# Performance work log

Measured on AMD Instinct MI355X. Metric: run time of the kernel, lower is better.

## Reference

```python
import jax, jax.numpy as jnp
import numpy as np

D_MODEL = 1024
N_HEADS = 16
N_GROUPS = 4
D_HEAD = D_MODEL // N_HEADS  # 64
HPG = N_HEADS // N_GROUPS    # heads per KV group = 4
B, T = 2, 2048


def _rope(x):
    # x: [B, H, T, D]; interleaved even/odd rotary, matching the torch module
    t, d = x.shape[2], x.shape[3]
    pos = jnp.arange(t, dtype=jnp.float32)[:, None]                      # [T,1]
    freq = jnp.exp(-(jnp.arange(0, d, 2, dtype=jnp.float32) / d)
                   * jnp.log(jnp.float32(10000.0)))                      # [D/2]
    angle = pos * freq                                                   # [T, D/2]
    cos, sin = jnp.cos(angle), jnp.sin(angle)
    xe, xo = x[..., ::2], x[..., 1::2]
    re = xe * cos - xo * sin
    ro = xe * sin + xo * cos
    return jnp.stack([re, ro], axis=-1).reshape(x.shape)


def setup_inputs() -> dict:
    key = jax.random.key(0)
    ks = jax.random.split(key, 10)
    s = 0.02
    return {
        "x":  jax.random.normal(ks[0], (B, T, D_MODEL), dtype=jnp.float32),
        "Wq": jax.random.normal(ks[1], (D_MODEL, D_MODEL), dtype=jnp.float32) * s,
        "bq": jax.random.normal(ks[2], (D_MODEL,), dtype=jnp.float32) * s,
        "Wk": jax.random.normal(ks[3], (D_MODEL, N_GROUPS * D_HEAD), dtype=jnp.float32) * s,
        "bk": jax.random.normal(ks[4], (N_GROUPS * D_HEAD,), dtype=jnp.float32) * s,
        "Wv": jax.random.normal(ks[5], (D_MODEL, N_GROUPS * D_HEAD), dtype=jnp.float32) * s,
        "bv": jax.random.normal(ks[6], (N_GROUPS * D_HEAD,), dtype=jnp.float32) * s,
        "Wo": jax.random.normal(ks[7], (D_MODEL, D_MODEL), dtype=jnp.float32) * s,
        "bo": jax.random.normal(ks[8], (D_MODEL,), dtype=jnp.float32) * s,
    }


def reference(x, Wq, bq, Wk, bk, Wv, bv, Wo, bo):
    b, t, _ = x.shape
    q = (x @ Wq + bq).reshape(b, t, N_HEADS, D_HEAD).transpose(0, 2, 1, 3)    # [B,H,T,D]
    k = (x @ Wk + bk).reshape(b, t, N_GROUPS, D_HEAD).transpose(0, 2, 1, 3)   # [B,G,T,D]
    v = (x @ Wv + bv).reshape(b, t, N_GROUPS, D_HEAD).transpose(0, 2, 1, 3)
    # GQA broadcast: idx = arange(n_heads) // heads_per_group  ==  repeat each group HPG times
    k = jnp.repeat(k, HPG, axis=1)                                            # [B,H,T,D]
    v = jnp.repeat(v, HPG, axis=1)
    q = _rope(q)
    k = _rope(k)
    scale = jnp.float32(np.sqrt(D_HEAD))
    scores = jnp.einsum('bhtd,bhsd->bhts', q, k) / scale                      # [B,H,T,T]
    causal = jnp.tril(jnp.ones((t, t), dtype=bool))
    scores = jnp.where(causal, scores, -jnp.inf)
    probs = jax.nn.softmax(scores, axis=-1)
    # dropout(p=0.05) is identity in eval mode
    attn = jnp.einsum('bhts,bhsd->bhtd', probs, v)
    out = attn.transpose(0, 2, 1, 3).reshape(b, t, N_HEADS * D_HEAD)
    return out @ Wo + bo
```

## Files before the change

### kernel.cpp

```cpp
#include <hip/hip_runtime.h>
#include <stdint.h>

typedef unsigned short u16;
typedef __attribute__((ext_vector_type(4))) float f32x4;
typedef __attribute__((ext_vector_type(8))) short bf16x8;
typedef __attribute__((ext_vector_type(4))) short bf16x4;

#define T_SEQ 2048
#define DM 1024
#define NH 16
#define NG 4
#define DH 64
#define QSCALE 0.18033688011112042f

__device__ __forceinline__ u16 f2bf(float f) {
    union { float f; uint32_t u; } v; v.f = f;
    uint32_t r = (v.u + 0x7FFFu + ((v.u >> 16) & 1u)) >> 16;
    return (u16)r;
}
__device__ __forceinline__ float bf2f(u16 u) {
    union { uint32_t u; float f; } v; v.u = ((uint32_t)u) << 16;
    return v.f;
}
__device__ __forceinline__ float fexp2(float x) {
#if __has_builtin(__builtin_amdgcn_exp2f)
    return __builtin_amdgcn_exp2f(x);
#else
    return exp2f(x);
#endif
}
__device__ __forceinline__ uint32_t cvtpk_bf16(float a, float b) {
    uint32_t r;
    asm("v_cvt_pk_bf16_f32 %0, %1, %2" : "=v"(r) : "v"(a), "v"(b));
    return r;
}

#if __has_builtin(__builtin_amdgcn_mfma_f32_16x16x16_bf16)
__device__ __forceinline__ f32x4 mfma16(bf16x4 a, bf16x4 b, f32x4 c) {
    return __builtin_amdgcn_mfma_f32_16x16x16_bf16(a, b, c, 0, 0, 0);
}
#elif __has_builtin(__builtin_amdgcn_mfma_f32_16x16x16bf16_1k)
__device__ __forceinline__ f32x4 mfma16(bf16x4 a, bf16x4 b, f32x4 c) {
    return __builtin_amdgcn_mfma_f32_16x16x16bf16_1k(a, b, c, 0, 0, 0);
}
#else
__device__ __forceinline__ f32x4 mfma16(bf16x4 a, bf16x4 b, f32x4 c) {
    asm("v_mfma_f32_16x16x16_bf16 %0, %1, %2, %0" : "+v"(c) : "v"(a), "v"(b));
    return c;
}
#endif

__device__ __forceinline__ void async16(const void* g, void* l) {
    __builtin_amdgcn_global_load_lds(
        (const __attribute__((address_space(1))) void*)g,
        (__attribute__((address_space(3))) void*)l,
        16, 0, 0);
}

__global__ __launch_bounds__(256) void k_prep(
    const float* __restrict__ x, u16* __restrict__ xb,
    const float* __restrict__ Wq, const float* __restrict__ Wk,
    const float* __restrict__ Wv, const float* __restrict__ Wo,
    u16* __restrict__ wqkvt, u16* __restrict__ wot,
    const float* __restrict__ bq, const float* __restrict__ bk,
    const float* __restrict__ bv, float* __restrict__ bqkv,
    float2* __restrict__ tbl) {
    int blk = blockIdx.x;
    int tid = threadIdx.x;
    if (blk < 2048) {
        int i = blk * 256 + tid;
        const float4* p = (const float4*)x + (size_t)i * 2;
        float4 a = p[0], b = p[1];
        bf16x8 v;
        v[0] = (short)f2bf(a.x); v[1] = (short)f2bf(a.y);
        v[2] = (short)f2bf(a.z); v[3] = (short)f2bf(a.w);
        v[4] = (short)f2bf(b.x); v[5] = (short)f2bf(b.y);
        v[6] = (short)f2bf(b.z); v[7] = (short)f2bf(b.w);
        ((bf16x8*)xb)[i] = v;
        return;
    }
    int t = blk - 2048;
    if (t >= 2560) {
        int u = t - 2560;
        if (u < 6) {
            int i = u * 256 + tid;
            if (i < 1536) {
                float v;
                if (i < 1024) v = bq[i];
                else if (i < 1280) v = bk[i - 1024];
                else v = bv[i - 1280];
                bqkv[i] = v;
            }
        } else {
            int idx = (u - 6) * 256 + tid;
            int tt = idx >> 5, i = idx & 31;
            float freq = exp2f(-(float)i * (13.287712379549449f / 32.0f));
            float ang = (float)tt * freq;
            tbl[idx] = make_float2(cosf(ang), sinf(ang));
        }
        return;
    }
    const float* src; u16* dst; int N;
    if (t < 1024)      { src = Wq; dst = wqkvt;                      N = 1024; }
    else if (t < 1280) { t -= 1024; src = Wk; dst = wqkvt + (size_t)1024 * 1024; N = 256; }
    else if (t < 1536) { t -= 1280; src = Wv; dst = wqkvt + (size_t)1280 * 1024; N = 256; }
    else               { t -= 1536; src = Wo; dst = wot;             N = 1024; }
    int ntiles = N >> 5;
    int n0 = (t % ntiles) * 32, k0 = (t / ntiles) * 32;
    __shared__ float tile[32][33];
    int tx = tid & 31, ty = tid >> 5;
#pragma unroll
    for (int q = 0; q < 4; q++)
        tile[ty + q * 8][tx] = src[(size_t)(k0 + ty + q * 8) * N + n0 + tx];
    __syncthreads();
#pragma unroll
    for (int q = 0; q < 4; q++)
        dst[(size_t)(n0 + ty + q * 8) * 1024 + k0 + tx] = f2bf(tile[tx][ty + q * 8]);
}

template <int EPI>
__global__ __launch_bounds__(256) void k_gemm(
    const u16* __restrict__ A, const u16* __restrict__ Bt,
    const float* __restrict__ bias, float* __restrict__ C,
    const float2* __restrict__ tbl, u16* __restrict__ Qo,
    u16* __restrict__ Ko, u16* __restrict__ Vto, int N, int K) {
    __shared__ __align__(16) u16 As[2][64 * 64];
    __shared__ __align__(16) u16 Bs[2][128 * 64];
    int tid = threadIdx.x;
    int lane = tid & 63, wid = tid >> 6;
    int wr = wid >> 1, wc = wid & 1;
    int l15 = lane & 15, lhi = lane >> 4;
    int row0 = blockIdx.y * 64, col0 = blockIdx.x * 128;
    f32x4 acc[2][4] = {};

    const u16* ga[2];
    const u16* gb[4];
#pragma unroll
    for (int i = 0; i < 2; i++) {
        int c = i * 256 + tid, r = c >> 3, sch = (c & 7) ^ (r & 7);
        ga[i] = A + (size_t)(row0 + r) * K + sch * 8;
    }
#pragma unroll
    for (int i = 0; i < 4; i++) {
        int c = i * 256 + tid, r = c >> 3, sch = (c & 7) ^ (r & 7);
        gb[i] = Bt + (size_t)(col0 + r) * K + sch * 8;
    }

#pragma unroll
    for (int i = 0; i < 2; i++) async16(ga[i], &As[0][(i * 256 + tid) * 8]);
#pragma unroll
    for (int i = 0; i < 4; i++) async16(gb[i], &Bs[0][(i * 256 + tid) * 8]);
    __syncthreads();

    int nk = K >> 6;
    for (int kt = 0; kt < nk; kt++) {
        int cur = kt & 1;
        if (kt + 1 < nk) {
            int nx = cur ^ 1, ko = (kt + 1) << 6;
#pragma unroll
            for (int i = 0; i < 2; i++) async16(ga[i] + ko, &As[nx][(i * 256 + tid) * 8]);
#pragma unroll
            for (int i = 0; i < 4; i++) async16(gb[i] + ko, &Bs[nx][(i * 256 + tid) * 8]);
        }
        const u16* Ac = As[cur];
        const u16* Bc = Bs[cur];
#pragma unroll
        for (int ks = 0; ks < 2; ks++) {
            bf16x8 af[2], bfr[4];
#pragma unroll
            for (int m = 0; m < 2; m++) {
                int r = wr * 32 + m * 16 + l15;
                int kb = (ks * 64 + lhi * 16) ^ ((r & 7) << 4);
                af[m] = *(const bf16x8*)((const char*)Ac + r * 128 + kb);
            }
#pragma unroll
            for (int n = 0; n < 4; n++) {
                int r = wc * 64 + n * 16 + l15;
                int kb = (ks * 64 + lhi * 16) ^ ((r & 7) << 4);
                bfr[n] = *(const bf16x8*)((const char*)Bc + r * 128 + kb);
            }
#pragma unroll
            for (int m = 0; m < 2; m++)
#pragma unroll
                for (int n = 0; n < 4; n++)
                    acc[m][n] = __builtin_amdgcn_mfma_f32_16x16x32_bf16(
                        af[m], bfr[n], acc[m][n], 0, 0, 0);
        }
        __syncthreads();
    }

    if (EPI == 0) {
#pragma unroll
        for (int n = 0; n < 4; n++) {
            int col = col0 + wc * 64 + n * 16 + l15;
            float bv = bias[col];
#pragma unroll
            for (int m = 0; m < 2; m++) {
                int row = row0 + wr * 32 + m * 16 + lhi * 4;
#pragma unroll
                for (int i = 0; i < 4; i++)
                    C[(size_t)(row + i) * N + col] = acc[m][n][i] + bv;
            }
        }
    } else {
        int type = (col0 >= 1280) ? 2 : (col0 >= 1024 ? 1 : 0);
        int rbase = row0 + wr * 32;
#pragma unroll
        for (int n = 0; n < 4; n++) {
            int col = col0 + wc * 64 + n * 16 + l15;
            float bv = bias[col];
            if (type == 2) {
                int cc = col - 1280;
                int g = cc >> 6, d = cc & 63;
#pragma unroll
                for (int m = 0; m < 2; m++)
#pragma unroll
                    for (int i = 0; i < 4; i++) {
                        int rowg = rbase + m * 16 + lhi * 4 + i;
                        int t = rowg & (T_SEQ - 1), b = rowg >> 11;
                        int sp = t ^ ((d & 1) << 2);
                        Vto[(((size_t)(b * NG + g)) * DH + d) * T_SEQ + sp] =
                            f2bf(acc[m][n][i] + bv);
                    }
            } else {
                float ssgn = (col & 1) ? 1.f : -1.f;
                int ip = (col & 63) >> 1;
#pragma unroll
                for (int m = 0; m < 2; m++)
#pragma unroll
                    for (int i = 0; i < 4; i++) {
                        int rowg = rbase + m * 16 + lhi * 4 + i;
                        int t = rowg & (T_SEQ - 1), b = rowg >> 11;
                        float v = acc[m][n][i] + bv;
                        float other = __shfl_xor(v, 1);
                        float2 cs = tbl[t * 32 + ip];
                        float out = v * cs.x + other * cs.y * ssgn;
                        if (type == 0) {
                            int h = col >> 6, d = col & 63;
                            Qo[(((size_t)(b * NH + h)) * T_SEQ + t) * DH + d] =
                                f2bf(out * QSCALE);
                        } else {
                            int cc = col - 1024;
                            int g = cc >> 6, d = cc & 63;
                            Ko[(((size_t)(b * NG + g)) * T_SEQ + t) * DH + d] = f2bf(out);
                        }
                    }
            }
        }
    }
}

__global__ __launch_bounds__(256) void k_attn(
    const u16* __restrict__ Q, const u16* __restrict__ K,
    const u16* __restrict__ Vt, u16* __restrict__ Aout) {
    int i0 = blockIdx.x;
    int u = i0 >> 5;
    int qt = (u < 16) ? (31 - u) : (u - 16);
    int bh = i0 & 31;
    int b = bh >> 4, h = bh & 15, g = h >> 2;
    int tid = threadIdx.x;
    int lane = tid & 63, wid = tid >> 6;
    int l15 = lane & 15, lhi = lane >> 4;

    const u16* Kp = K + ((size_t)(b * NG + g)) * T_SEQ * DH;
    const u16* Vp = Vt + ((size_t)(b * NG + g)) * DH * T_SEQ;

    __shared__ __align__(16) u16 Ks[2][64 * 64];
    __shared__ __align__(16) u16 Vs[2][64 * 64];

    const u16* Qp = Q + ((size_t)bh * T_SEQ + qt * 64) * DH;
    bf16x8 qf[2];
#pragma unroll
    for (int ks = 0; ks < 2; ks++)
        qf[ks] = *(const bf16x8*)(Qp + (size_t)(wid * 16 + l15) * DH + ks * 32 + lhi * 8);

    f32x4 of[4] = {};
    float m_i = -3.0e38f, l_i = 0.f;

    int nt = qt + 1;
    int swz = (l15 & 7) << 4;

    int c0 = tid, c1 = tid + 256;
    int rk0 = c0 >> 3, rk1 = c1 >> 3;
    int sk0 = (c0 & 7) ^ (rk0 & 7);
    int sk1 = (c1 & 7) ^ (rk1 & 7);
    int sv0 = (c0 & 7) ^ ((rk0 >> 1) & 7);
    int sv1 = (c1 & 7) ^ ((rk1 >> 1) & 7);
    const u16* kg0 = Kp + rk0 * DH + sk0 * 8;
    const u16* kg1 = Kp + rk1 * DH + sk1 * 8;
    const u16* vg0 = Vp + (size_t)rk0 * T_SEQ + sv0 * 8;
    const u16* vg1 = Vp + (size_t)rk1 * T_SEQ + sv1 * 8;

    async16(kg0, &Ks[0][c0 * 8]);
    async16(kg1, &Ks[0][c1 * 8]);
    async16(vg0, &Vs[0][c0 * 8]);
    async16(vg1, &Vs[0][c1 * 8]);
    __syncthreads();

#pragma unroll 1
    for (int it = 0; it < nt; it++) {
        int cur = it & 1;
        if (it + 1 < nt) {
            int nx = cur ^ 1;
            int ko = (it + 1) << 12;
            int vo = (it + 1) << 6;
            async16(kg0 + ko, &Ks[nx][c0 * 8]);
            async16(kg1 + ko, &Ks[nx][c1 * 8]);
            async16(vg0 + vo, &Vs[nx][c0 * 8]);
            async16(vg1 + vo, &Vs[nx][c1 * 8]);
        }
        const u16* Kc = Ks[cur];
        const u16* Vc = Vs[cur];

        f32x4 sf[4] = {};
        __builtin_amdgcn_s_setprio(1);
#pragma unroll
        for (int ks = 0; ks < 2; ks++)
#pragma unroll
            for (int n = 0; n < 4; n++) {
                int kb = (ks * 64 + lhi * 16) ^ swz;
                bf16x8 kf = *(const bf16x8*)((const char*)Kc + (n * 16 + l15) * 128 + kb);
                sf[n] = __builtin_amdgcn_mfma_f32_16x16x32_bf16(kf, qf[ks], sf[n], 0, 0, 0);
            }
        __builtin_amdgcn_s_setprio(0);

        if (it == nt - 1) {
            int qrow = qt * 64 + wid * 16 + l15;
            int sb = it * 64 + lhi * 4;
#pragma unroll
            for (int n = 0; n < 4; n++)
#pragma unroll
                for (int i = 0; i < 4; i++)
                    if (sb + n * 16 + i > qrow) sf[n][i] = -3.0e38f;
        }

        float pmt = sf[0][0];
#pragma unroll
        for (int n = 0; n < 4; n++)
#pragma unroll
            for (int i = 0; i < 4; i++)
                pmt = fmaxf(pmt, sf[n][i]);
        if (!__all(pmt - m_i <= 8.f)) {
#pragma unroll
            for (int off = 16; off <= 32; off <<= 1)
                pmt = fmaxf(pmt, __shfl_xor(pmt, off));
            float mn = fmaxf(m_i, pmt);
            float sc = fexp2(m_i - mn);
            m_i = mn;
            l_i *= sc;
            float sc4[4];
#pragma unroll
            for (int i = 0; i < 4; i++)
                sc4[i] = __shfl(sc, lhi * 4 + i);
#pragma unroll
            for (int n = 0; n < 4; n++)
#pragma unroll
                for (int i = 0; i < 4; i++)
                    of[n][i] *= sc4[i];
        }
        bf16x4 pa[4];
#pragma unroll
        for (int n = 0; n < 4; n++) {
#pragma unroll
            for (int i = 0; i < 4; i++) {
                float p = fexp2(sf[n][i] - m_i);
                sf[n][i] = p;
                l_i += p;
            }
            union { uint32_t uu[2]; bf16x4 v; } pu;
            pu.uu[0] = cvtpk_bf16(sf[n][0], sf[n][1]);
            pu.uu[1] = cvtpk_bf16(sf[n][2], sf[n][3]);
            pa[n] = pu.v;
        }

        __builtin_amdgcn_s_setprio(1);
#pragma unroll
        for (int nd = 0; nd < 4; nd++) {
            int rowb = (nd * 16 + l15) * 128;
#pragma unroll
            for (int n = 0; n < 4; n++) {
                int kb = ((4 * n + lhi) ^ l15) << 3;
                bf16x4 vf = *(const bf16x4*)((const char*)Vc + rowb + kb);
                of[nd] = mfma16(pa[n], vf, of[nd]);
            }
        }
        __builtin_amdgcn_s_setprio(0);
        __syncthreads();
    }

#pragma unroll
    for (int off = 16; off <= 32; off <<= 1)
        l_i += __shfl_xor(l_i, off);
    float lq[4];
#pragma unroll
    for (int i = 0; i < 4; i++)
        lq[i] = __shfl(l_i, lhi * 4 + i);
#pragma unroll
    for (int n = 0; n < 4; n++)
#pragma unroll
        for (int i = 0; i < 4; i++) {
            int trow = qt * 64 + wid * 16 + lhi * 4 + i;
            float v = of[n][i] / lq[i];
            Aout[((size_t)(b * T_SEQ + trow)) * DM + h * 64 + n * 16 + l15] = f2bf(v);
        }
}

extern "C" void kernel_launch(void* const* d_in, const int* in_sizes, int n_in,
                              void* d_out, int out_size, void* d_ws, size_t ws_size,
                              hipStream_t stream) {
    const float* x  = (const float*)d_in[0];
    const float* Wq = (const float*)d_in[1];
    const float* bq = (const float*)d_in[2];
    const float* Wk = (const float*)d_in[3];
    const float* bk = (const float*)d_in[4];
    const float* Wv = (const float*)d_in[5];
    const float* bv = (const float*)d_in[6];
    const float* Wo = (const float*)d_in[7];
    const float* bo = (const float*)d_in[8];

    char* ws = (char*)d_ws;
    size_t o = 0;
    u16*   xb    = (u16*)(ws + o);  o += (size_t)4096 * 1024 * 2;
    u16*   wqkvt = (u16*)(ws + o);  o += (size_t)1536 * 1024 * 2;
    u16*   wot   = (u16*)(ws + o);  o += (size_t)1024 * 1024 * 2;
    float* bqkv  = (float*)(ws + o); o += 1536 * 4;
    o = (o + 255) & ~(size_t)255;
    u16*   Qb    = (u16*)(ws + o);  o += (size_t)2 * NH * T_SEQ * DH * 2;
    u16*   Kb    = (u16*)(ws + o);  o += (size_t)2 * NG * T_SEQ * DH * 2;
    u16*   Vtb   = (u16*)(ws + o);  o += (size_t)2 * NG * DH * T_SEQ * 2;
    u16*   attnb = (u16*)(ws + o);  o += (size_t)4096 * 1024 * 2;
    float2* tbl  = (float2*)(ws + o); o += (size_t)2048 * 32 * 8;

    k_prep<<<4870, 256, 0, stream>>>(x, xb, Wq, Wk, Wv, Wo, wqkvt, wot, bq, bk, bv, bqkv, tbl);
    k_gemm<1><<<dim3(12, 64), 256, 0, stream>>>(xb, wqkvt, bqkv, nullptr, tbl, Qb, Kb, Vtb, 1536, 1024);
    k_attn<<<1024, 256, 0, stream>>>(Qb, Kb, Vtb, attnb);
    k_gemm<0><<<dim3(8, 64), 256, 0, stream>>>(attnb, wot, bo, (float*)d_out, nullptr, nullptr, nullptr, nullptr, 1024, 1024);
}
```

Measured before the change: 90.98 us.

## Software-pipeline QK^T of next tile with softmax/PV of current tile

```diff
diff --git a/kernel.cpp b/kernel.cpp
--- a/kernel.cpp
+++ b/kernel.cpp
@@ -266,7 +266,7 @@
     const u16* Vp = Vt + ((size_t)(b * NG + g)) * DH * T_SEQ;
 
     __shared__ __align__(16) u16 Ks[2][64 * 64];
-    __shared__ __align__(16) u16 Vs[2][64 * 64];
+    __shared__ __align__(16) u16 Vs[3][64 * 64];
 
     const u16* Qp = Q + ((size_t)bh * T_SEQ + qt * 64) * DH;
     bf16x8 qf[2];
@@ -296,42 +296,38 @@
     async16(vg0, &Vs[0][c0 * 8]);
     async16(vg1, &Vs[0][c1 * 8]);
     __syncthreads();
+    if (nt > 1) {
+        async16(kg0 + (1 << 12), &Ks[1][c0 * 8]);
+        async16(kg1 + (1 << 12), &Ks[1][c1 * 8]);
+        async16(vg0 + (1 << 6), &Vs[1][c0 * 8]);
+        async16(vg1 + (1 << 6), &Vs[1][c1 * 8]);
+    }
+    f32x4 sf[4] = {};
+    __builtin_amdgcn_s_setprio(1);
+#pragma unroll
+    for (int ks = 0; ks < 2; ks++)
+#pragma unroll
+        for (int n = 0; n < 4; n++) {
+            int kb = (ks * 64 + lhi * 16) ^ swz;
+            bf16x8 kf = *(const bf16x8*)((const char*)Ks[0] + (n * 16 + l15) * 128 + kb);
+            sf[n] = __builtin_amdgcn_mfma_f32_16x16x32_bf16(kf, qf[ks], sf[n], 0, 0, 0);
+        }
+    __builtin_amdgcn_s_setprio(0);
+    __syncthreads();
+
+    u16* vread = Vs[0];
+    u16* vhold = Vs[1];
+    u16* vstage = Vs[2];
 
 #pragma unroll 1
-    for (int it = 0; it < nt; it++) {
-        int cur = it & 1;
+    for (int it = 1; it < nt; it++) {
         if (it + 1 < nt) {
-            int nx = cur ^ 1;
-            int ko = (it + 1) << 12;
-            int vo = (it + 1) << 6;
+            int ko = (it + 1) << 12, vo = (it + 1) << 6;
+            int nx = (it + 1) & 1;
             async16(kg0 + ko, &Ks[nx][c0 * 8]);
             async16(kg1 + ko, &Ks[nx][c1 * 8]);
-            async16(vg0 + vo, &Vs[nx][c0 * 8]);
-            async16(vg1 + vo, &Vs[nx][c1 * 8]);
-        }
-        const u16* Kc = Ks[cur];
-        const u16* Vc = Vs[cur];
-
-        f32x4 sf[4] = {};
-        __builtin_amdgcn_s_setprio(1);
-#pragma unroll
-        for (int ks = 0; ks < 2; ks++)
-#pragma unroll
-            for (int n = 0; n < 4; n++) {
-                int kb = (ks * 64 + lhi * 16) ^ swz;
-                bf16x8 kf = *(const bf16x8*)((const char*)Kc + (n * 16 + l15) * 128 + kb);
-                sf[n] = __builtin_amdgcn_mfma_f32_16x16x32_bf16(kf, qf[ks], sf[n], 0, 0, 0);
-            }
-        __builtin_amdgcn_s_setprio(0);
-
-        if (it == nt - 1) {
-            int qrow = qt * 64 + wid * 16 + l15;
-            int sb = it * 64 + lhi * 4;
-#pragma unroll
-            for (int n = 0; n < 4; n++)
-#pragma unroll
-                for (int i = 0; i < 4; i++)
-                    if (sb + n * 16 + i > qrow) sf[n][i] = -3.0e38f;
+            async16(vg0 + vo, vstage + c0 * 8);
+            async16(vg1 + vo, vstage + c1 * 8);
         }
 
         float pmt = sf[0][0];
@@ -373,19 +369,92 @@
             pa[n] = pu.v;
         }
 
+        const u16* Kc = Ks[it & 1];
         __builtin_amdgcn_s_setprio(1);
+#pragma unroll
+        for (int ks = 0; ks < 2; ks++)
+#pragma unroll
+            for (int n = 0; n < 4; n++) {
+                int kb = (ks * 64 + lhi * 16) ^ swz;
+                bf16x8 kf = *(const bf16x8*)((const char*)Kc + (n * 16 + l15) * 128 + kb);
+                f32x4 z = (ks == 0) ? f32x4{0.f, 0.f, 0.f, 0.f} : sf[n];
+                sf[n] = __builtin_amdgcn_mfma_f32_16x16x32_bf16(kf, qf[ks], z, 0, 0, 0);
+            }
+
 #pragma unroll
         for (int nd = 0; nd < 4; nd++) {
             int rowb = (nd * 16 + l15) * 128;
 #pragma unroll
             for (int n = 0; n < 4; n++) {
                 int kb = ((4 * n + lhi) ^ l15) << 3;
-                bf16x4 vf = *(const bf16x4*)((const char*)Vc + rowb + kb);
+                bf16x4 vf = *(const bf16x4*)((const char*)vread + rowb + kb);
                 of[nd] = mfma16(pa[n], vf, of[nd]);
             }
         }
         __builtin_amdgcn_s_setprio(0);
+
+        u16* tmp = vread; vread = vhold; vhold = vstage; vstage = tmp;
         __syncthreads();
+    }
+
+    {
+        int qrow = qt * 64 + wid * 16 + l15;
+        int sb = (nt - 1) * 64 + lhi * 4;
+#pragma unroll
+        for (int n = 0; n < 4; n++)
+#pragma unroll
+            for (int i = 0; i < 4; i++)
+                if (sb + n * 16 + i > qrow) sf[n][i] = -3.0e38f;
+        float pmt = sf[0][0];
+#pragma unroll
+        for (int n = 0; n < 4; n++)
+#pragma unroll
+            for (int i = 0; i < 4; i++)
+                pmt = fmaxf(pmt, sf[n][i]);
+        if (!__all(pmt - m_i <= 8.f)) {
+#pragma unroll
+            for (int off = 16; off <= 32; off <<= 1)
+                pmt = fmaxf(pmt, __shfl_xor(pmt, off));
+            float mn = fmaxf(m_i, pmt);
+            float sc = fexp2(m_i - mn);
+            m_i = mn;
+            l_i *= sc;
+            float sc4[4];
+#pragma unroll
+            for (int i = 0; i < 4; i++)
+                sc4[i] = __shfl(sc, lhi * 4 + i);
+#pragma unroll
+            for (int n = 0; n < 4; n++)
+#pragma unroll
+                for (int i = 0; i < 4; i++)
+                    of[n][i] *= sc4[i];
+        }
+        bf16x4 pa[4];
+#pragma unroll
+        for (int n = 0; n < 4; n++) {
+#pragma unroll
+            for (int i = 0; i < 4; i++) {
+                float p = fexp2(sf[n][i] - m_i);
+                sf[n][i] = p;
+                l_i += p;
+            }
+            union { uint32_t uu[2]; bf16x4 v; } pu;
+            pu.uu[0] = cvtpk_bf16(sf[n][0], sf[n][1]);
+            pu.uu[1] = cvtpk_bf16(sf[n][2], sf[n][3]);
+            pa[n] = pu.v;
+        }
+        __builtin_amdgcn_s_setprio(1);
+#pragma unroll
+        for (int nd = 0; nd < 4; nd++) {
+            int rowb = (nd * 16 + l15) * 128;
+#pragma unroll
+            for (int n = 0; n < 4; n++) {
+                int kb = ((4 * n + lhi) ^ l15) << 3;
+                bf16x4 vf = *(const bf16x4*)((const char*)vread + rowb + kb);
+                of[nd] = mfma16(pa[n], vf, of[nd]);
+            }
+        }
+        __builtin_amdgcn_s_setprio(0);
     }
 
 #pragma unroll
```

Measured after the change: 88.58 us. 2.6% less time.
